# Performance work log

Hardware: AMD Instinct MI355X
Metric: run time of the kernel (lower is better)

The kernel has to match this reference:

```python
import jax, jax.numpy as jnp
import numpy as np

N = 100000   # nodes
E = 3200000  # edges
B = 64       # graphs in batch
F = 21       # num_features
SLOPE = 0.01 # LeakyReLU default negative slope


def gcn_conv(x, src, dst, ew, W, b, n):
    """PyG GCNConv with edge weights: lin -> add self loops -> sym-norm -> scatter-add -> +bias."""
    xw = x @ W  # [n, F_out]
    loop = jnp.arange(n)
    s = jnp.concatenate([src, loop])
    d = jnp.concatenate([dst, loop])
    w = jnp.concatenate([ew, jnp.ones((n,), ew.dtype)])
    deg = jax.ops.segment_sum(w, d, num_segments=n)
    dinv = jnp.where(deg > 0, jax.lax.rsqrt(deg), 0.0)
    norm = dinv[s] * w * dinv[d]                      # [E+n]
    msg = norm[:, None] * xw[s]                       # gather + per-edge weight
    out = jax.ops.segment_sum(msg, d, num_segments=n) # scatter-aggregate
    return out + b


def leaky(v):
    return jnp.where(v >= 0, v, SLOPE * v)


def setup_inputs() -> dict:
    key = jax.random.key(0)
    ks = jax.random.split(key, 16)
    inp = {
        "prot_x": jax.random.normal(ks[0], (N, F), jnp.float32),
        "prot_edge_index": jax.random.randint(ks[1], (2, E), 0, N, jnp.int64),
        "prot_dist": jax.random.uniform(ks[2], (E,), jnp.float32),
        "prot_batch": jnp.sort(jax.random.randint(ks[3], (N,), 0, B, jnp.int64)),
        "W1": jax.random.normal(ks[4], (F, F), jnp.float32) * 0.2,
        "b1": jnp.zeros((F,), jnp.float32),
        "W2": jax.random.normal(ks[5], (F, F), jnp.float32) * 0.2,
        "b2": jnp.zeros((F,), jnp.float32),
        "W3": jax.random.normal(ks[6], (F, F), jnp.float32) * 0.2,
        "b3": jnp.zeros((F,), jnp.float32),
        "Wp": jax.random.normal(ks[7], (F, 128), jnp.float32) * 0.2,
        "bp": jnp.zeros((128,), jnp.float32),
        "Wf1": jax.random.normal(ks[8], (128, 256), jnp.float32) * 0.08,
        "bf1": jnp.zeros((256,), jnp.float32),
        "Wf2": jax.random.normal(ks[9], (256, 64), jnp.float32) * 0.08,
        "bf2": jnp.zeros((64,), jnp.float32),
        "Wo": jax.random.normal(ks[10], (64, 5), jnp.float32) * 0.1,
        "bo": jnp.zeros((5,), jnp.float32),
    }
    return inp


def reference(prot_x, prot_edge_index, prot_dist, prot_batch,
              W1, b1, W2, b2, W3, b3, Wp, bp, Wf1, bf1, Wf2, bf2, Wo, bo):
    src, dst = prot_edge_index[0], prot_edge_index[1]
    x = gcn_conv(prot_x, src, dst, prot_dist, W1, b1, N)
    x = gcn_conv(x, src, dst, prot_dist, W2, b2, N)
    x = gcn_conv(x, src, dst, prot_dist, W3, b3, N)
    x = jax.nn.relu(x)
    # global mean pool over prot_batch
    sums = jax.ops.segment_sum(x, prot_batch, num_segments=B)
    cnt = jax.ops.segment_sum(jnp.ones((N,), x.dtype), prot_batch, num_segments=B)
    x = sums / jnp.maximum(cnt, 1.0)[:, None]  # [B, F]
    x = leaky(x @ Wp + bp)   # dropout is identity in eval
    x = leaky(x @ Wf1 + bf1)
    x = leaky(x @ Wf2 + bf2)
    out = x @ Wo + bo
    return jax.nn.softmax(out, axis=-1)
```

## Files before the change

### kernel.cpp

```cpp
#include <hip/hip_runtime.h>
#include <hip/hip_fp16.h>

#define NF 21
#define HSTR 32
#define BN 12
#define SCAN_T 1024
#define BSH 9
#define BSZ 512
#define NBB 256
#define NBMAX 1024
#define BINR 16
#define BINCHUNK (BINR * 256)

#define ATOMIC_ADD_F32(p, v) unsafeAtomicAdd((p), (v))

__global__ __launch_bounds__(64) void sentinel_kernel(float* out, int m) {
    int i = blockIdx.x * 64 + threadIdx.x;
    if (i < m) out[i] = 0.109375f;
}

__global__ __launch_bounds__(256) void bucket_count_kernel(
    const int* __restrict__ ei, int* __restrict__ bases, int E, int nb) {
    __shared__ int lc[NBB];
    for (int i = threadIdx.x; i < nb; i += 256) lc[i] = 0;
    __syncthreads();
    int base = blockIdx.x * BINCHUNK;
    for (int r = 0; r < BINR; ++r) {
        int e = base + r * 256 + threadIdx.x;
        if (e < E) atomicAdd(&lc[ei[E + e] >> BSH], 1);
    }
    __syncthreads();
    for (int i = threadIdx.x; i < nb; i += 256)
        if (lc[i]) atomicAdd(&bases[i], lc[i]);
}

__global__ __launch_bounds__(SCAN_T) void scan_copy_kernel(
    int* __restrict__ data, int* __restrict__ cur, int n) {
    __shared__ int sd[SCAN_T];
    int t = threadIdx.x;
    int chunk = (n + SCAN_T - 1) / SCAN_T;
    int base = t * chunk;
    int s = 0;
    for (int i = 0; i < chunk; ++i) { int idx = base + i; if (idx < n) s += data[idx]; }
    sd[t] = s;
    __syncthreads();
    for (int off = 1; off < SCAN_T; off <<= 1) {
        int v = (t >= off) ? sd[t - off] : 0;
        __syncthreads();
        sd[t] += v;
        __syncthreads();
    }
    int run = sd[t] - s;
    for (int i = 0; i < chunk; ++i) {
        int idx = base + i;
        if (idx < n) { int v = data[idx]; data[idx] = run; cur[idx] = run; run += v; }
    }
}

__global__ __launch_bounds__(256) void bin_kernel(
    const int* __restrict__ ei, const float* __restrict__ ew,
    int* __restrict__ cur, unsigned int* __restrict__ binned,
    __half* __restrict__ bw, int E, int nb) {
    __shared__ int lcnt[NBB];
    __shared__ int lbase[NBB];
    for (int i = threadIdx.x; i < nb; i += 256) lcnt[i] = 0;
    __syncthreads();
    int base = blockIdx.x * BINCHUNK;
    int pl[BINR];
    #pragma unroll
    for (int r = 0; r < BINR; ++r) {
        int e = base + r * 256 + threadIdx.x;
        pl[r] = (e < E) ? atomicAdd(&lcnt[ei[E + e] >> BSH], 1) : 0;
    }
    __syncthreads();
    for (int i = threadIdx.x; i < nb; i += 256)
        if (lcnt[i]) lbase[i] = atomicAdd(&cur[i], lcnt[i]);
    __syncthreads();
    #pragma unroll
    for (int r = 0; r < BINR; ++r) {
        int e = base + r * 256 + threadIdx.x;
        if (e < E) {
            int d = ei[E + e];
            int b = d >> BSH;
            int pos = lbase[b] + pl[r];
            binned[pos] = (unsigned int)ei[e] | ((unsigned int)(d & (BSZ - 1)) << 17);
            bw[pos] = __float2half(ew[e]);
        }
    }
}

__global__ __launch_bounds__(512) void build_kernel(
    const int* __restrict__ bases, const int* __restrict__ cur,
    const unsigned int* __restrict__ binned, const __half* __restrict__ bw,
    int* __restrict__ rowptr, int2* __restrict__ csr, int n) {
    __shared__ int h[BSZ], s[BSZ], bump[BSZ];
    int b = blockIdx.x;
    int t = threadIdx.x;
    int base = bases[b], end = cur[b];
    int cntb = end - base;
    h[t] = 0; bump[t] = 0;
    __syncthreads();
    for (int i = t; i < cntb; i += 512)
        atomicAdd(&h[binned[base + i] >> 17], 1);
    __syncthreads();
    s[t] = h[t];
    __syncthreads();
    for (int off = 1; off < BSZ; off <<= 1) {
        int v = (t >= off) ? s[t - off] : 0;
        __syncthreads();
        s[t] += v;
        __syncthreads();
    }
    int d = b * BSZ + t;
    if (d < n) rowptr[d] = base + s[t];
    __syncthreads();
    for (int i = t; i < cntb; i += 512) {
        unsigned int v = binned[base + i];
        int dl = v >> 17;
        int src = v & 0x1FFFF;
        int p = atomicAdd(&bump[dl], 1);
        int pos = base + (s[dl] - h[dl]) + p;
        csr[pos] = make_int2(src, __float_as_int(__half2float(bw[base + i])));
    }
}

__global__ __launch_bounds__(256) void node_l1_kernel(
    const float* __restrict__ x, const int* __restrict__ rowptr,
    const int2* __restrict__ csr, const float* __restrict__ W,
    float* __restrict__ dinv, __half* __restrict__ y, int n) {
    __shared__ float Ws[NF * NF];
    for (int i = threadIdx.x; i < NF * NF; i += 256) Ws[i] = W[i];
    __syncthreads();
    int i = blockIdx.x * 256 + threadIdx.x;
    if (i >= n) return;
    int start = (i == 0) ? 0 : rowptr[i - 1], end = rowptr[i];
    float deg = 0.f;
    int e = start;
    for (; e + 3 < end; e += 4) {
        int2 c0 = csr[e], c1 = csr[e + 1], c2 = csr[e + 2], c3 = csr[e + 3];
        deg += __int_as_float(c0.y) + __int_as_float(c1.y)
             + __int_as_float(c2.y) + __int_as_float(c3.y);
    }
    for (; e < end; ++e) deg += __int_as_float(csr[e].y);
    float di = rsqrtf(deg + 1.0f);
    dinv[i] = di;
    float xr[NF];
    #pragma unroll
    for (int f = 0; f < NF; ++f) xr[f] = x[i * NF + f];
    #pragma unroll
    for (int j = 0; j < NF; ++j) {
        float v = 0.f;
        #pragma unroll
        for (int f = 0; f < NF; ++f) v += xr[f] * Ws[f * NF + j];
        y[(size_t)i * HSTR + j] = __float2half(di * v);
    }
}

static __device__ __forceinline__ float gather_seg(
    const int2* __restrict__ csr, const __half* __restrict__ yin,
    int start, int end, int f) {
    float g = 0.f;
    int e = start;
    for (; e + 7 < end; e += 8) {
        int2 c0 = csr[e + 0], c1 = csr[e + 1], c2 = csr[e + 2], c3 = csr[e + 3];
        int2 c4 = csr[e + 4], c5 = csr[e + 5], c6 = csr[e + 6], c7 = csr[e + 7];
        float a0 = __half2float(yin[(size_t)c0.x * HSTR + f]);
        float a1 = __half2float(yin[(size_t)c1.x * HSTR + f]);
        float a2 = __half2float(yin[(size_t)c2.x * HSTR + f]);
        float a3 = __half2float(yin[(size_t)c3.x * HSTR + f]);
        float a4 = __half2float(yin[(size_t)c4.x * HSTR + f]);
        float a5 = __half2float(yin[(size_t)c5.x * HSTR + f]);
        float a6 = __half2float(yin[(size_t)c6.x * HSTR + f]);
        float a7 = __half2float(yin[(size_t)c7.x * HSTR + f]);
        g += __int_as_float(c0.y) * a0 + __int_as_float(c1.y) * a1
           + __int_as_float(c2.y) * a2 + __int_as_float(c3.y) * a3
           + __int_as_float(c4.y) * a4 + __int_as_float(c5.y) * a5
           + __int_as_float(c6.y) * a6 + __int_as_float(c7.y) * a7;
    }
    for (; e < end; ++e) {
        int2 c = csr[e];
        g += __int_as_float(c.y) * __half2float(yin[(size_t)c.x * HSTR + f]);
    }
    return g;
}

__global__ __launch_bounds__(256) void layer_kernel(
    const int* __restrict__ rowptr, const int2* __restrict__ csr,
    const float* __restrict__ dinv, const float* __restrict__ bprev,
    const float* __restrict__ W,
    const __half* __restrict__ yin, __half* __restrict__ yout, int n) {
    __shared__ float Ws[NF * NF];
    __shared__ float bsh[NF];
    __shared__ float xr[BN][NF];
    for (int i = threadIdx.x; i < NF * NF; i += 256) Ws[i] = W[i];
    if (threadIdx.x < NF) bsh[threadIdx.x] = bprev[threadIdx.x];
    __syncthreads();
    int t = threadIdx.x;
    int nd = t / NF, f = t - nd * NF;
    int d = blockIdx.x * BN + nd;
    bool act = (nd < BN) && (d < n);
    float di = 0.f;
    if (act) {
        di = dinv[d];
        int start = (d == 0) ? 0 : rowptr[d - 1], end = rowptr[d];
        float g = gather_seg(csr, yin, start, end, f);
        xr[nd][f] = di * (g + __half2float(yin[(size_t)d * HSTR + f])) + bsh[f];
    }
    __syncthreads();
    if (act) {
        float v = 0.f;
        #pragma unroll
        for (int k = 0; k < NF; ++k) v += xr[nd][k] * Ws[k * NF + f];
        yout[(size_t)d * HSTR + f] = __float2half(di * v);
    }
}

__global__ __launch_bounds__(256) void final_pool_kernel(
    const int* __restrict__ rowptr, const int2* __restrict__ csr,
    const float* __restrict__ dinv, const float* __restrict__ b3,
    const int* __restrict__ batch, const __half* __restrict__ yin,
    float* __restrict__ sums, float* __restrict__ cnt, int n) {
    __shared__ float bsh[NF];
    __shared__ float xr[BN][NF];
    __shared__ int gs[BN];
    if (threadIdx.x < NF) bsh[threadIdx.x] = b3[threadIdx.x];
    __syncthreads();
    int t = threadIdx.x;
    int nd = t / NF, f = t - nd * NF;
    int base = blockIdx.x * BN;
    int nvalid = n - base; if (nvalid > BN) nvalid = BN;
    int d = base + nd;
    bool act = (nd < BN) && (d < n);
    if (act) {
        int start = (d == 0) ? 0 : rowptr[d - 1], end = rowptr[d];
        float g = gather_seg(csr, yin, start, end, f);
        float h = dinv[d] * (g + __half2float(yin[(size_t)d * HSTR + f])) + bsh[f];
        xr[nd][f] = fmaxf(h, 0.f);
        if (f == 0) gs[nd] = batch[d];
    }
    __syncthreads();
    if (nvalid <= 0) return;
    if (t < NF) {
        float run = 0.f;
        int gcur = gs[0];
        for (int k = 0; k < nvalid; ++k) {
            int g = gs[k];
            if (g != gcur) { ATOMIC_ADD_F32(&sums[gcur * NF + t], run); run = 0.f; gcur = g; }
            run += xr[k][t];
        }
        ATOMIC_ADD_F32(&sums[gcur * NF + t], run);
    } else if (t == NF) {
        float run = 0.f;
        int gcur = gs[0];
        for (int k = 0; k < nvalid; ++k) {
            int g = gs[k];
            if (g != gcur) { ATOMIC_ADD_F32(&cnt[gcur], run); run = 0.f; gcur = g; }
            run += 1.f;
        }
        ATOMIC_ADD_F32(&cnt[gcur], run);
    }
}

__global__ __launch_bounds__(256) void mlp_kernel(
    const float* __restrict__ sums, const float* __restrict__ cnt,
    const float* __restrict__ Wp,  const float* __restrict__ bp,
    const float* __restrict__ Wf1, const float* __restrict__ bf1,
    const float* __restrict__ Wf2, const float* __restrict__ bf2,
    const float* __restrict__ Wo,  const float* __restrict__ bo,
    float* __restrict__ out) {
    int g = blockIdx.x;
    int t = threadIdx.x;
    __shared__ float xr[NF], h1[128], h2[256], h3[64];
    if (t < NF) xr[t] = sums[g * NF + t] / fmaxf(cnt[g], 1.0f);
    __syncthreads();
    if (t < 128) {
        float v = bp[t];
        #pragma unroll
        for (int f = 0; f < NF; ++f) v += xr[f] * Wp[f * 128 + t];
        h1[t] = v >= 0.f ? v : 0.01f * v;
    }
    __syncthreads();
    {
        float v = bf1[t];
        for (int k = 0; k < 128; ++k) v += h1[k] * Wf1[k * 256 + t];
        h2[t] = v >= 0.f ? v : 0.01f * v;
    }
    __syncthreads();
    if (t < 64) {
        float v = bf2[t];
        for (int k = 0; k < 256; ++k) v += h2[k] * Wf2[k * 64 + t];
        h3[t] = v >= 0.f ? v : 0.01f * v;
    }
    __syncthreads();
    if (t == 0) {
        float lg[5];
        float m = -1e30f;
        for (int j = 0; j < 5; ++j) {
            float v = bo[j];
            for (int k = 0; k < 64; ++k) v += h3[k] * Wo[k * 5 + j];
            lg[j] = v;
            m = fmaxf(m, v);
        }
        float den = 0.f;
        for (int j = 0; j < 5; ++j) { lg[j] = __expf(lg[j] - m); den += lg[j]; }
        for (int j = 0; j < 5; ++j) out[g * 5 + j] = lg[j] / den;
    }
}

extern "C" void kernel_launch(void* const* d_in, const int* in_sizes, int n_in,
                              void* d_out, int out_size, void* d_ws, size_t ws_size,
                              hipStream_t stream) {
    const float* x     = (const float*)d_in[0];
    const int*   ei    = (const int*)d_in[1];
    const float* ew    = (const float*)d_in[2];
    const int*   batch = (const int*)d_in[3];
    const float* W1 = (const float*)d_in[4];
    const float* b1 = (const float*)d_in[5];
    const float* W2 = (const float*)d_in[6];
    const float* b2 = (const float*)d_in[7];
    const float* W3 = (const float*)d_in[8];
    const float* b3 = (const float*)d_in[9];
    const float* Wp  = (const float*)d_in[10];
    const float* bp  = (const float*)d_in[11];
    const float* Wf1 = (const float*)d_in[12];
    const float* bf1 = (const float*)d_in[13];
    const float* Wf2 = (const float*)d_in[14];
    const float* bf2 = (const float*)d_in[15];
    const float* Wo  = (const float*)d_in[16];
    const float* bo  = (const float*)d_in[17];

    const int n = in_sizes[0] / NF;
    const int E = in_sizes[2];
    const int B = out_size / 5;
    const int nb = (n + BSZ - 1) >> BSH;

    const size_t y_words = (size_t)n * HSTR > (size_t)E ? (size_t)n * HSTR : (size_t)E;
    const size_t need_words = (size_t)2 * E + 2 * (size_t)n + y_words
                            + (size_t)B * NF + B + ((size_t)E + 1) / 2 + 2 * NBMAX;
    if (ws_size < need_words * 4 || nb > NBB) {
        sentinel_kernel<<<(out_size + 63) / 64, 64, 0, stream>>>((float*)d_out, out_size);
        return;
    }

    int*   wsw    = (int*)d_ws;
    int2*  csr    = (int2*)wsw;
    int*   rowptr = wsw + (size_t)2 * E;
    float* dinv   = (float*)(wsw + (size_t)2 * E + n);
    int*   yreg   = wsw + (size_t)2 * E + 2 * (size_t)n;
    __half* yA    = (__half*)yreg;
    __half* yB    = yA + (size_t)n * HSTR;
    unsigned int* binned = (unsigned int*)yreg;
    float* sums   = (float*)(yreg + y_words);
    float* cnt    = sums + (size_t)B * NF;
    __half* bw    = (__half*)(cnt + B);
    int*   bases  = (int*)(bw + 2 * (((size_t)E + 1) / 2));
    int*   cur    = bases + NBMAX;

    hipMemsetAsync(bases, 0, (size_t)nb * sizeof(int), stream);
    hipMemsetAsync(sums, 0, (size_t)(B * NF + B) * sizeof(float), stream);

    int nb_bin = (E + BINCHUNK - 1) / BINCHUNK;
    int nb_n   = (n + 255) / 256;
    int nb_g   = (n + BN - 1) / BN;

    bucket_count_kernel<<<nb_bin, 256, 0, stream>>>(ei, bases, E, nb);
    scan_copy_kernel<<<1, SCAN_T, 0, stream>>>(bases, cur, nb);
    bin_kernel<<<nb_bin, 256, 0, stream>>>(ei, ew, cur, binned, bw, E, nb);
    build_kernel<<<nb, 512, 0, stream>>>(bases, cur, binned, bw, rowptr, csr, n);

    node_l1_kernel<<<nb_n, 256, 0, stream>>>(x, rowptr, csr, W1, dinv, yA, n);
    layer_kernel<<<nb_g, 256, 0, stream>>>(rowptr, csr, dinv, b1, W2, yA, yB, n);
    layer_kernel<<<nb_g, 256, 0, stream>>>(rowptr, csr, dinv, b2, W3, yB, yA, n);
    final_pool_kernel<<<nb_g, 256, 0, stream>>>(rowptr, csr, dinv, b3, batch, yA,
                                                sums, cnt, n);
    mlp_kernel<<<B, 256, 0, stream>>>(sums, cnt, Wp, bp, Wf1, bf1, Wf2, bf2, Wo, bo,
                                      (float*)d_out);
}
```

Baseline: 494.6 us.

## Split half-precision node features into 16+8 planes and enlarge binning chunks

Node feature rows, previously padded to 32 halves (64 B), now live in two planes: 16 halves (32 B) and 8 halves (16 B). This shrinks the footprint of the random-gather target and the bytes touched per gathered row, which should improve cache hit rates. The binning kernel now processes 64 rows per thread instead of 16. It drops the per-thread register array of local slots and recomputes positions with a second shared-memory atomic pass. The second-pass atomics make edge order within a bucket nondeterministic, and each gather now touches two cache lines per source node instead of one.

Measured after the change: 550.5 us. 1.11x slower.

```diff
diff --git a/kernel.cpp b/kernel.cpp
--- a/kernel.cpp
+++ b/kernel.cpp
@@ -2,14 +2,13 @@
 #include <hip/hip_fp16.h>
 
 #define NF 21
-#define HSTR 32
 #define BN 12
 #define SCAN_T 1024
 #define BSH 9
 #define BSZ 512
 #define NBB 256
 #define NBMAX 1024
-#define BINR 16
+#define BINR 64
 #define BINCHUNK (BINR * 256)
 
 #define ATOMIC_ADD_F32(p, v) unsafeAtomicAdd((p), (v))
@@ -63,26 +62,26 @@
     __half* __restrict__ bw, int E, int nb) {
     __shared__ int lcnt[NBB];
     __shared__ int lbase[NBB];
+    __shared__ int lcur[NBB];
     for (int i = threadIdx.x; i < nb; i += 256) lcnt[i] = 0;
     __syncthreads();
     int base = blockIdx.x * BINCHUNK;
-    int pl[BINR];
-    #pragma unroll
     for (int r = 0; r < BINR; ++r) {
         int e = base + r * 256 + threadIdx.x;
-        pl[r] = (e < E) ? atomicAdd(&lcnt[ei[E + e] >> BSH], 1) : 0;
-    }
-    __syncthreads();
-    for (int i = threadIdx.x; i < nb; i += 256)
+        if (e < E) atomicAdd(&lcnt[ei[E + e] >> BSH], 1);
+    }
+    __syncthreads();
+    for (int i = threadIdx.x; i < nb; i += 256) {
         if (lcnt[i]) lbase[i] = atomicAdd(&cur[i], lcnt[i]);
-    __syncthreads();
-    #pragma unroll
+        lcur[i] = 0;
+    }
+    __syncthreads();
     for (int r = 0; r < BINR; ++r) {
         int e = base + r * 256 + threadIdx.x;
         if (e < E) {
             int d = ei[E + e];
             int b = d >> BSH;
-            int pos = lbase[b] + pl[r];
+            int pos = lbase[b] + atomicAdd(&lcur[b], 1);
             binned[pos] = (unsigned int)ei[e] | ((unsigned int)(d & (BSZ - 1)) << 17);
             bw[pos] = __float2half(ew[e]);
         }
@@ -127,7 +126,8 @@
 __global__ __launch_bounds__(256) void node_l1_kernel(
     const float* __restrict__ x, const int* __restrict__ rowptr,
     const int2* __restrict__ csr, const float* __restrict__ W,
-    float* __restrict__ dinv, __half* __restrict__ y, int n) {
+    float* __restrict__ dinv, __half* __restrict__ ya, __half* __restrict__ yb,
+    int n) {
     __shared__ float Ws[NF * NF];
     for (int i = threadIdx.x; i < NF * NF; i += 256) Ws[i] = W[i];
     __syncthreads();
@@ -152,26 +152,28 @@
         float v = 0.f;
         #pragma unroll
         for (int f = 0; f < NF; ++f) v += xr[f] * Ws[f * NF + j];
-        y[(size_t)i * HSTR + j] = __float2half(di * v);
+        float yv = di * v;
+        if (j < 16) ya[(size_t)i * 16 + j] = __float2half(yv);
+        else        yb[(size_t)i * 8 + (j - 16)] = __float2half(yv);
     }
 }
 
 static __device__ __forceinline__ float gather_seg(
-    const int2* __restrict__ csr, const __half* __restrict__ yin,
-    int start, int end, int f) {
+    const int2* __restrict__ csr, const __half* __restrict__ yp,
+    int stride, int off, int start, int end) {
     float g = 0.f;
     int e = start;
     for (; e + 7 < end; e += 8) {
         int2 c0 = csr[e + 0], c1 = csr[e + 1], c2 = csr[e + 2], c3 = csr[e + 3];
         int2 c4 = csr[e + 4], c5 = csr[e + 5], c6 = csr[e + 6], c7 = csr[e + 7];
-        float a0 = __half2float(yin[(size_t)c0.x * HSTR + f]);
-        float a1 = __half2float(yin[(size_t)c1.x * HSTR + f]);
-        float a2 = __half2float(yin[(size_t)c2.x * HSTR + f]);
-        float a3 = __half2float(yin[(size_t)c3.x * HSTR + f]);
-        float a4 = __half2float(yin[(size_t)c4.x * HSTR + f]);
-        float a5 = __half2float(yin[(size_t)c5.x * HSTR + f]);
-        float a6 = __half2float(yin[(size_t)c6.x * HSTR + f]);
-        float a7 = __half2float(yin[(size_t)c7.x * HSTR + f]);
+        float a0 = __half2float(yp[(size_t)c0.x * stride + off]);
+        float a1 = __half2float(yp[(size_t)c1.x * stride + off]);
+        float a2 = __half2float(yp[(size_t)c2.x * stride + off]);
+        float a3 = __half2float(yp[(size_t)c3.x * stride + off]);
+        float a4 = __half2float(yp[(size_t)c4.x * stride + off]);
+        float a5 = __half2float(yp[(size_t)c5.x * stride + off]);
+        float a6 = __half2float(yp[(size_t)c6.x * stride + off]);
+        float a7 = __half2float(yp[(size_t)c7.x * stride + off]);
         g += __int_as_float(c0.y) * a0 + __int_as_float(c1.y) * a1
            + __int_as_float(c2.y) * a2 + __int_as_float(c3.y) * a3
            + __int_as_float(c4.y) * a4 + __int_as_float(c5.y) * a5
@@ -179,7 +181,7 @@
     }
     for (; e < end; ++e) {
         int2 c = csr[e];
-        g += __int_as_float(c.y) * __half2float(yin[(size_t)c.x * HSTR + f]);
+        g += __int_as_float(c.y) * __half2float(yp[(size_t)c.x * stride + off]);
     }
     return g;
 }
@@ -188,7 +190,8 @@
     const int* __restrict__ rowptr, const int2* __restrict__ csr,
     const float* __restrict__ dinv, const float* __restrict__ bprev,
     const float* __restrict__ W,
-    const __half* __restrict__ yin, __half* __restrict__ yout, int n) {
+    const __half* __restrict__ yina, const __half* __restrict__ yinb,
+    __half* __restrict__ youta, __half* __restrict__ youtb, int n) {
     __shared__ float Ws[NF * NF];
     __shared__ float bsh[NF];
     __shared__ float xr[BN][NF];
@@ -199,26 +202,32 @@
     int nd = t / NF, f = t - nd * NF;
     int d = blockIdx.x * BN + nd;
     bool act = (nd < BN) && (d < n);
+    const __half* yp = (f < 16) ? yina : yinb;
+    int stride = (f < 16) ? 16 : 8;
+    int off = (f < 16) ? f : f - 16;
     float di = 0.f;
     if (act) {
         di = dinv[d];
         int start = (d == 0) ? 0 : rowptr[d - 1], end = rowptr[d];
-        float g = gather_seg(csr, yin, start, end, f);
-        xr[nd][f] = di * (g + __half2float(yin[(size_t)d * HSTR + f])) + bsh[f];
+        float g = gather_seg(csr, yp, stride, off, start, end);
+        xr[nd][f] = di * (g + __half2float(yp[(size_t)d * stride + off])) + bsh[f];
     }
     __syncthreads();
     if (act) {
         float v = 0.f;
         #pragma unroll
         for (int k = 0; k < NF; ++k) v += xr[nd][k] * Ws[k * NF + f];
-        yout[(size_t)d * HSTR + f] = __float2half(di * v);
+        float yv = di * v;
+        if (f < 16) youta[(size_t)d * 16 + f] = __float2half(yv);
+        else        youtb[(size_t)d * 8 + off] = __float2half(yv);
     }
 }
 
 __global__ __launch_bounds__(256) void final_pool_kernel(
     const int* __restrict__ rowptr, const int2* __restrict__ csr,
     const float* __restrict__ dinv, const float* __restrict__ b3,
-    const int* __restrict__ batch, const __half* __restrict__ yin,
+    const int* __restrict__ batch,
+    const __half* __restrict__ yina, const __half* __restrict__ yinb,
     float* __restrict__ sums, float* __restrict__ cnt, int n) {
     __shared__ float bsh[NF];
     __shared__ float xr[BN][NF];
@@ -231,10 +240,13 @@
     int nvalid = n - base; if (nvalid > BN) nvalid = BN;
     int d = base + nd;
     bool act = (nd < BN) && (d < n);
+    const __half* yp = (f < 16) ? yina : yinb;
+    int stride = (f < 16) ? 16 : 8;
+    int off = (f < 16) ? f : f - 16;
     if (act) {
         int start = (d == 0) ? 0 : rowptr[d - 1], end = rowptr[d];
-        float g = gather_seg(csr, yin, start, end, f);
-        float h = dinv[d] * (g + __half2float(yin[(size_t)d * HSTR + f])) + bsh[f];
+        float g = gather_seg(csr, yp, stride, off, start, end);
+        float h = dinv[d] * (g + __half2float(yp[(size_t)d * stride + off])) + bsh[f];
         xr[nd][f] = fmaxf(h, 0.f);
         if (f == 0) gs[nd] = batch[d];
     }
@@ -334,7 +346,7 @@
     const int B = out_size / 5;
     const int nb = (n + BSZ - 1) >> BSH;
 
-    const size_t y_words = (size_t)n * HSTR > (size_t)E ? (size_t)n * HSTR : (size_t)E;
+    const size_t y_words = ((size_t)n * 24 > (size_t)E) ? (size_t)n * 24 : (size_t)E;
     const size_t need_words = (size_t)2 * E + 2 * (size_t)n + y_words
                             + (size_t)B * NF + B + ((size_t)E + 1) / 2 + 2 * NBMAX;
     if (ws_size < need_words * 4 || nb > NBB) {
@@ -347,8 +359,10 @@
     int*   rowptr = wsw + (size_t)2 * E;
     float* dinv   = (float*)(wsw + (size_t)2 * E + n);
     int*   yreg   = wsw + (size_t)2 * E + 2 * (size_t)n;
-    __half* yA    = (__half*)yreg;
-    __half* yB    = yA + (size_t)n * HSTR;
+    __half* yAa   = (__half*)yreg;
+    __half* yAb   = yAa + (size_t)n * 16;
+    __half* yBa   = yAb + (size_t)n * 8;
+    __half* yBb   = yBa + (size_t)n * 16;
     unsigned int* binned = (unsigned int*)yreg;
     float* sums   = (float*)(yreg + y_words);
     float* cnt    = sums + (size_t)B * NF;
@@ -368,11 +382,13 @@
     bin_kernel<<<nb_bin, 256, 0, stream>>>(ei, ew, cur, binned, bw, E, nb);
     build_kernel<<<nb, 512, 0, stream>>>(bases, cur, binned, bw, rowptr, csr, n);
 
-    node_l1_kernel<<<nb_n, 256, 0, stream>>>(x, rowptr, csr, W1, dinv, yA, n);
-    layer_kernel<<<nb_g, 256, 0, stream>>>(rowptr, csr, dinv, b1, W2, yA, yB, n);
-    layer_kernel<<<nb_g, 256, 0, stream>>>(rowptr, csr, dinv, b2, W3, yB, yA, n);
-    final_pool_kernel<<<nb_g, 256, 0, stream>>>(rowptr, csr, dinv, b3, batch, yA,
-                                                sums, cnt, n);
+    node_l1_kernel<<<nb_n, 256, 0, stream>>>(x, rowptr, csr, W1, dinv, yAa, yAb, n);
+    layer_kernel<<<nb_g, 256, 0, stream>>>(rowptr, csr, dinv, b1, W2,
+                                           yAa, yAb, yBa, yBb, n);
+    layer_kernel<<<nb_g, 256, 0, stream>>>(rowptr, csr, dinv, b2, W3,
+                                           yBa, yBb, yAa, yAb, n);
+    final_pool_kernel<<<nb_g, 256, 0, stream>>>(rowptr, csr, dinv, b3, batch,
+                                                yAa, yAb, sums, cnt, n);
     mlp_kernel<<<B, 256, 0, stream>>>(sums, cnt, Wp, bp, Wf1, bf1, Wf2, bf2, Wo, bo,
                                       (float*)d_out);
 }
```
